# Kernel tuning notes

Hardware: AMD Instinct MI355X
Metric: run time of the kernel (lower is better)

## Reference

```python
import jax, jax.numpy as jnp
import numpy as np

N, C, H, W = 8, 32, 16, 16   # input batch / channels / spatial
OC = 64                       # out_channels
K = 3                         # kernel_size
PAD = 1                       # padding (stride=1, dilation=1 -> output HxW == input HxW)
WIDTH = 8                     # hwcfg['width']
RLEN = 2 ** WIDTH             # Sobol RNG sequence length = 256
CKK = C * K * K               # unfolded patch length = 288
B = N * H * W                 # flattened patch batch = 2048


def _sobol_rng():
    # 1-D Sobol sequence == van der Corput base-2: bit-reversed counter scaled to [0, 2^width)
    idx = np.arange(RLEN, dtype=np.uint32)
    rev = np.zeros(RLEN, dtype=np.uint32)
    for b in range(WIDTH):
        rev |= ((idx >> b) & 1) << (WIDTH - 1 - b)
    return jnp.asarray(rev.astype(np.float32))


def setup_inputs() -> dict:
    key = jax.random.key(0)
    k1, k2, k3, k4, k5, k6 = jax.random.split(key, 6)
    # unary (stochastic bitstream) input: bits in {0,1}
    x = jax.random.bernoulli(k1, 0.5, (N, C, H, W)).astype(jnp.float32)
    # BinGen, bipolar: binary = round((v + 1)/2 * 2^width), v in [-1, 1]
    w = jax.random.uniform(k2, (OC, CKK), minval=-1.0, maxval=1.0)
    w_bin = jnp.round((w + 1.0) / 2.0 * RLEN)
    b = jax.random.uniform(k3, (OC,), minval=-1.0, maxval=1.0)
    b_bin = jnp.round((b + 1.0) / 2.0 * RLEN)
    rng = _sobol_rng()
    # mid-stream BSGen index state (per patch position, as the module cats to batch copies)
    wrdx_i1 = jax.random.randint(k4, (B, OC, CKK), 0, RLEN, dtype=jnp.int32)
    wrdx_i0 = jax.random.randint(k5, (B, OC, CKK), 0, RLEN, dtype=jnp.int32)
    brdx = jax.random.randint(k6, (OC,), 0, RLEN, dtype=jnp.int32)
    return {"x": x, "w_bin": w_bin, "b_bin": b_bin, "rng": rng,
            "wrdx_i1": wrdx_i1, "wrdx_i0": wrdx_i0, "brdx": brdx}


def _unfold(x):
    # even cycle -> ConstantPad2d(pad, 0); torch.nn.functional.unfold ordering (c, kh, kw)
    xp = jnp.pad(x, ((0, 0), (0, 0), (PAD, PAD), (PAD, PAD)))
    cols = jnp.stack([xp[:, :, i:i + H, j:j + W] for i in range(K) for j in range(K)], axis=2)
    # [N, C, K*K, H, W] -> [N, CKK, L] -> [N, L, CKK] -> [B, CKK]
    return cols.reshape(N, CKK, H * W).transpose(0, 2, 1).reshape(B, CKK)


def reference(x, w_bin, b_bin, rng, wrdx_i1, wrdx_i0, brdx):
    ib1 = _unfold(x)                                                        # [B, CKK], bits
    # BSGen: bit = (binary_value > rng[index % RLEN])
    wbit1 = (w_bin[None] > rng[wrdx_i1 % RLEN]).astype(jnp.float32)         # [B, OC, CKK]
    wbit0 = 1.0 - (w_bin[None] > rng[wrdx_i0 % RLEN]).astype(jnp.float32)   # [B, OC, CKK]
    # bipolar parallel counter: x*w1 path + (1-x)*(1-w) path
    obin = (jnp.einsum('bk,bok->bo', ib1, wbit1)
            + jnp.einsum('bk,bok->bo', 1.0 - ib1, wbit0))                   # [B, OC]
    bbit = (b_bin > rng[brdx % RLEN]).astype(jnp.float32)                   # [OC]
    # fold(1,1): [N, L, OC] -> [N, OC, H, W]
    out = obin.reshape(N, H * W, OC).transpose(0, 2, 1).reshape(N, OC, H, W)
    return out + bbit[None, :, None, None]
```

## Files before the change

kernel.cpp:

```cpp
#include <hip/hip_runtime.h>


#define CH   32
#define HH   16
#define WW   16
#define OCN  64
#define CKK  288
#define LL   256
#define BB   2048

__device__ __forceinline__ float sobol_val(int idx) {
    return (float)(__brev((unsigned)idx) >> 24);
}

__device__ __forceinline__ float contrib(float xb, float wv, int i1, int i0) {
    float t1  = (wv > sobol_val(i1)) ? 1.f : 0.f;
    float nt0 = (wv > sobol_val(i0)) ? 0.f : 1.f;
    return (xb != 0.f) ? t1 : nt0;
}

__global__ __launch_bounds__(256) void fsuconv_kernel(
    const float* __restrict__ x,
    const float* __restrict__ w_bin,
    const float* __restrict__ b_bin,
    const int*   __restrict__ wrdx1,
    const int*   __restrict__ wrdx0,
    const int*   __restrict__ brdx,
    float*       __restrict__ out)
{
    __shared__ __align__(16) float ib1[CKK];

    const int blk = blockIdx.x;
    const int b   = blk >> 4;
    const int og  = blk & 15;
    const int n   = b >> 8;
    const int l   = b & 255;
    const int h   = l >> 4;
    const int w0  = l & 15;

    for (int k = threadIdx.x; k < CKK; k += 256) {
        int c  = k / 9;
        int r  = k - c * 9;
        int kh = r / 3;
        int kw = r - kh * 3;
        int ih = h + kh - 1;
        int iw = w0 + kw - 1;
        float v = 0.f;
        if ((unsigned)ih < 16u && (unsigned)iw < 16u)
            v = x[((n * CH + c) * HH + ih) * WW + iw];
        ib1[k] = v;
    }
    __syncthreads();

    const int wave = threadIdx.x >> 6;
    const int lane = threadIdx.x & 63;
    const int o    = og * 4 + wave;

    const size_t rowoff = ((size_t)b * OCN + o) * CKK;
    const int4*   r1 = (const int4*)(wrdx1 + rowoff);
    const int4*   r0 = (const int4*)(wrdx0 + rowoff);
    const float4* wr = (const float4*)(w_bin + (size_t)o * CKK);

    float sum = 0.f;

    {
        int4   a  = r1[lane];
        int4   c0 = r0[lane];
        float4 wv = wr[lane];
        float4 xv = *(const float4*)&ib1[lane * 4];
        sum += contrib(xv.x, wv.x, a.x, c0.x);
        sum += contrib(xv.y, wv.y, a.y, c0.y);
        sum += contrib(xv.z, wv.z, a.z, c0.z);
        sum += contrib(xv.w, wv.w, a.w, c0.w);
    }
    if (lane < 8) {
        int4   a  = r1[64 + lane];
        int4   c0 = r0[64 + lane];
        float4 wv = wr[64 + lane];
        float4 xv = *(const float4*)&ib1[256 + lane * 4];
        sum += contrib(xv.x, wv.x, a.x, c0.x);
        sum += contrib(xv.y, wv.y, a.y, c0.y);
        sum += contrib(xv.z, wv.z, a.z, c0.z);
        sum += contrib(xv.w, wv.w, a.w, c0.w);
    }

    for (int off = 32; off > 0; off >>= 1)
        sum += __shfl_down(sum, off);

    if (lane == 0) {
        float bb = (b_bin[o] > sobol_val(brdx[o])) ? 1.f : 0.f;
        out[((size_t)n * OCN + o) * LL + l] = sum + bb;
    }
}

extern "C" void kernel_launch(void* const* d_in, const int* in_sizes, int n_in,
                              void* d_out, int out_size, void* d_ws, size_t ws_size,
                              hipStream_t stream) {
    const float* x     = (const float*)d_in[0];
    const float* w_bin = (const float*)d_in[1];
    const float* b_bin = (const float*)d_in[2];
    const int*   wrdx1 = (const int*)d_in[4];
    const int*   wrdx0 = (const int*)d_in[5];
    const int*   brdx  = (const int*)d_in[6];
    float*       out   = (float*)d_out;

    dim3 grid(BB * 16);
    dim3 block(256);
    fsuconv_kernel<<<grid, block, 0, stream>>>(x, w_bin, b_bin, wrdx1, wrdx0, brdx, out);
}
```

Baseline: 316.6 us.

## Precompute unfolded input masks and integer weights, batch index loads per wave

Adds a prep kernel that writes the unfolded input as integer masks and the weights as integer thresholds into workspace. The main kernel then maps eight output channels to each wave, eight lanes per channel, and issues all nine int4 loads of both index streams up front before doing the branchless integer compare. The intent is to raise memory-level parallelism on the dominant streaming reads of the two index tensors and to drop the per-block shared-memory unfold and barrier. The cost is an extra launch plus workspace traffic, and lanes now read strided int4 chunks, which may change coalescing.

```diff
diff --git a/kernel.cpp b/kernel.cpp
--- a/kernel.cpp
+++ b/kernel.cpp
@@ -9,87 +9,94 @@
 #define LL   256
 #define BB   2048
 
-__device__ __forceinline__ float sobol_val(int idx) {
-    return (float)(__brev((unsigned)idx) >> 24);
+__global__ __launch_bounds__(256) void prep_kernel(
+    const float* __restrict__ x,
+    const float* __restrict__ w_bin,
+    int* __restrict__ xm,
+    int* __restrict__ w1m,
+    int* __restrict__ w0c)
+{
+    int e = blockIdx.x * 256 + threadIdx.x;
+    if (e < BB * CKK) {
+        int b = e / CKK, k = e - b * CKK;
+        int c = k / 9,  r = k - c * 9;
+        int kh = r / 3, kw = r - kh * 3;
+        int n = b >> 8, l = b & 255, h = l >> 4, w0 = l & 15;
+        int ih = h + kh - 1, iw = w0 + kw - 1;
+        float v = 0.f;
+        if ((unsigned)ih < 16u && (unsigned)iw < 16u)
+            v = x[((n * CH + c) * HH + ih) * WW + iw];
+        xm[e] = (v != 0.f) ? -1 : 0;
+    } else {
+        int e2 = e - BB * CKK;
+        if (e2 < OCN * CKK) {
+            int wi = (int)w_bin[e2];
+            w1m[e2] = wi - 1;
+            w0c[e2] = 255 - wi;
+        }
+    }
 }
 
-__device__ __forceinline__ float contrib(float xb, float wv, int i1, int i0) {
-    float t1  = (wv > sobol_val(i1)) ? 1.f : 0.f;
-    float nt0 = (wv > sobol_val(i0)) ? 0.f : 1.f;
-    return (xb != 0.f) ? t1 : nt0;
+__device__ __forceinline__ int elem(int i1, int i0, int m, int u, int v) {
+    int ni0 = ~i0;
+    int I  = ni0 ^ ((i1 ^ ni0) & m);
+    int Wp = v   ^ ((u  ^ v)  & m);
+    int t  = (int)(__brev((unsigned)I) >> 24);
+    return (t <= Wp) ? 1 : 0;
 }
 
-__global__ __launch_bounds__(256) void fsuconv_kernel(
-    const float* __restrict__ x,
-    const float* __restrict__ w_bin,
-    const float* __restrict__ b_bin,
+__global__ __launch_bounds__(256, 4) void fsu_main(
     const int*   __restrict__ wrdx1,
     const int*   __restrict__ wrdx0,
+    const int*   __restrict__ xm,
+    const int*   __restrict__ w1m,
+    const int*   __restrict__ w0c,
+    const float* __restrict__ b_bin,
     const int*   __restrict__ brdx,
     float*       __restrict__ out)
 {
-    __shared__ __align__(16) float ib1[CKK];
+    const int wid  = (blockIdx.x << 2) + (threadIdx.x >> 6);
+    const int lane = threadIdx.x & 63;
+    const int b    = wid >> 3;
+    const int og   = wid & 7;
+    const int g    = lane >> 3;
+    const int j    = lane & 7;
+    const int o    = (og << 3) + g;
 
-    const int blk = blockIdx.x;
-    const int b   = blk >> 4;
-    const int og  = blk & 15;
-    const int n   = b >> 8;
-    const int l   = b & 255;
-    const int h   = l >> 4;
-    const int w0  = l & 15;
+    const int4* r1 = (const int4*)(wrdx1 + ((size_t)b * OCN + o) * CKK);
+    const int4* r0 = (const int4*)(wrdx0 + ((size_t)b * OCN + o) * CKK);
+    const int4* xr = (const int4*)(xm  + (size_t)b * CKK);
+    const int4* wa = (const int4*)(w1m + (size_t)o * CKK);
+    const int4* wb = (const int4*)(w0c + (size_t)o * CKK);
 
-    for (int k = threadIdx.x; k < CKK; k += 256) {
-        int c  = k / 9;
-        int r  = k - c * 9;
-        int kh = r / 3;
-        int kw = r - kh * 3;
-        int ih = h + kh - 1;
-        int iw = w0 + kw - 1;
-        float v = 0.f;
-        if ((unsigned)ih < 16u && (unsigned)iw < 16u)
-            v = x[((n * CH + c) * HH + ih) * WW + iw];
-        ib1[k] = v;
-    }
-    __syncthreads();
-
-    const int wave = threadIdx.x >> 6;
-    const int lane = threadIdx.x & 63;
-    const int o    = og * 4 + wave;
-
-    const size_t rowoff = ((size_t)b * OCN + o) * CKK;
-    const int4*   r1 = (const int4*)(wrdx1 + rowoff);
-    const int4*   r0 = (const int4*)(wrdx0 + rowoff);
-    const float4* wr = (const float4*)(w_bin + (size_t)o * CKK);
-
-    float sum = 0.f;
-
-    {
-        int4   a  = r1[lane];
-        int4   c0 = r0[lane];
-        float4 wv = wr[lane];
-        float4 xv = *(const float4*)&ib1[lane * 4];
-        sum += contrib(xv.x, wv.x, a.x, c0.x);
-        sum += contrib(xv.y, wv.y, a.y, c0.y);
-        sum += contrib(xv.z, wv.z, a.z, c0.z);
-        sum += contrib(xv.w, wv.w, a.w, c0.w);
-    }
-    if (lane < 8) {
-        int4   a  = r1[64 + lane];
-        int4   c0 = r0[64 + lane];
-        float4 wv = wr[64 + lane];
-        float4 xv = *(const float4*)&ib1[256 + lane * 4];
-        sum += contrib(xv.x, wv.x, a.x, c0.x);
-        sum += contrib(xv.y, wv.y, a.y, c0.y);
-        sum += contrib(xv.z, wv.z, a.z, c0.z);
-        sum += contrib(xv.w, wv.w, a.w, c0.w);
+    int4 A1[9], A0[9];
+#pragma unroll
+    for (int t = 0; t < 9; ++t) {
+        A1[t] = r1[j + (t << 3)];
+        A0[t] = r0[j + (t << 3)];
     }
 
-    for (int off = 32; off > 0; off >>= 1)
-        sum += __shfl_down(sum, off);
+    int cnt = 0;
+#pragma unroll
+    for (int t = 0; t < 9; ++t) {
+        const int c = j + (t << 3);
+        int4 m = xr[c];
+        int4 u = wa[c];
+        int4 v = wb[c];
+        cnt += elem(A1[t].x, A0[t].x, m.x, u.x, v.x);
+        cnt += elem(A1[t].y, A0[t].y, m.y, u.y, v.y);
+        cnt += elem(A1[t].z, A0[t].z, m.z, u.z, v.z);
+        cnt += elem(A1[t].w, A0[t].w, m.w, u.w, v.w);
+    }
 
-    if (lane == 0) {
-        float bb = (b_bin[o] > sobol_val(brdx[o])) ? 1.f : 0.f;
-        out[((size_t)n * OCN + o) * LL + l] = sum + bb;
+    cnt += __shfl_down(cnt, 4);
+    cnt += __shfl_down(cnt, 2);
+    cnt += __shfl_down(cnt, 1);
+
+    if (j == 0) {
+        int n = b >> 8, l = b & 255;
+        float bb = (b_bin[o] > (float)(__brev((unsigned)brdx[o]) >> 24)) ? 1.f : 0.f;
+        out[((size_t)n * OCN + o) * LL + l] = (float)cnt + bb;
     }
 }
 
@@ -104,7 +111,18 @@
     const int*   brdx  = (const int*)d_in[6];
     float*       out   = (float*)d_out;
 
-    dim3 grid(BB * 16);
-    dim3 block(256);
-    fsuconv_kernel<<<grid, block, 0, stream>>>(x, w_bin, b_bin, wrdx1, wrdx0, brdx, out);
+    int* xm  = (int*)d_ws;
+    int* w1m = xm  + BB * CKK;
+    int* w0c = w1m + OCN * CKK;
+
+    {
+        int total = BB * CKK + OCN * CKK;
+        dim3 grid((total + 255) / 256), block(256);
+        prep_kernel<<<grid, block, 0, stream>>>(x, w_bin, xm, w1m, w0c);
+    }
+    {
+        dim3 grid(BB * 8 / 4), block(256);
+        fsu_main<<<grid, block, 0, stream>>>(wrdx1, wrdx0, xm, w1m, w0c,
+                                             b_bin, brdx, out);
+    }
 }
```

New measurement: 321.5 us. About the same (+1.6%).
